# Kernel tuning notes

Hardware: AMD Instinct MI355X
Metric: run time of the kernel (lower is better)

The kernel has to match this reference:

```python
import jax, jax.numpy as jnp
import numpy as np

C = 512
NUM_GROUPS = 32
EPS = 1e-6


def setup_inputs() -> dict:
    key = jax.random.key(0)
    ks = jax.random.split(key, 6)
    B, H, W = 4, 64, 64
    x = jax.random.normal(ks[0], (B, H, W, C), dtype=jnp.float32)
    # GroupNorm affine params (flax default init: scale=1, bias=0)
    gn_scale = jnp.ones((C,), jnp.float32)
    gn_bias = jnp.zeros((C,), jnp.float32)
    # 1x1 convs == per-pixel dense layers; weight [C_in, C_out], bias [C_out]
    def dense(k):
        return jax.random.normal(k, (C, C), dtype=jnp.float32) * 0.02
    wq, wk, wv, wo = dense(ks[1]), dense(ks[2]), dense(ks[3]), dense(ks[4])
    bq = jnp.zeros((C,), jnp.float32)
    bk = jnp.zeros((C,), jnp.float32)
    bv = jnp.zeros((C,), jnp.float32)
    bo = jnp.zeros((C,), jnp.float32)
    return {"x": x, "gn_scale": gn_scale, "gn_bias": gn_bias,
            "wq": wq, "bq": bq, "wk": wk, "bk": bk,
            "wv": wv, "bv": bv, "wo": wo, "bo": bo}


def _group_norm(x, scale, bias):
    B, H, W, Cc = x.shape
    g = NUM_GROUPS
    xg = x.reshape(B, H, W, g, Cc // g)
    mean = jnp.mean(xg, axis=(1, 2, 4), keepdims=True)
    var = jnp.var(xg, axis=(1, 2, 4), keepdims=True)
    xn = (xg - mean) * jax.lax.rsqrt(var + EPS)
    xn = xn.reshape(B, H, W, Cc)
    return xn * scale + bias


def reference(x, gn_scale, gn_bias, wq, bq, wk, bk, wv, bv, wo, bo):
    B, H, W, Cc = x.shape
    hn = _group_norm(x, gn_scale, gn_bias)
    # 1x1 convs
    q = (hn @ wq + bq).reshape(B, H * W, Cc)
    k = (hn @ wk + bk).reshape(B, H * W, Cc)
    v = (hn @ wv + bv).reshape(B, H * W, Cc)
    scale = jnp.asarray(Cc, x.dtype) ** -0.5
    # scores[b,i,j] = <q_i, k_j> * c^-0.5; softmax over keys j
    attn = jax.nn.softmax(jnp.einsum('bic,bjc->bij', q, k) * scale, axis=-1)
    out = jnp.einsum('bij,bjc->bic', attn, v).reshape(B, H, W, Cc)
    return x + (out @ wo + bo)
```

## Files before the change

kernel.cpp:

```cpp
#include <hip/hip_runtime.h>


typedef __attribute__((ext_vector_type(8))) __bf16 bf16x8;
typedef __attribute__((ext_vector_type(4))) __bf16 bf16x4;
typedef __attribute__((ext_vector_type(4))) float  floatx4;

#define C_DIM 512
#define SPB   4096
#define MTOT  16384

#define HN_OFF  ((size_t)0)
#define Q_OFF   ((size_t)16 << 20)
#define K_OFF   ((size_t)32 << 20)
#define V4_OFF  ((size_t)48 << 20)
#define WT_OFF  ((size_t)64 << 20)
#define O1_OFF  ((size_t)68 << 20)
#define ML_OFF  ((size_t)84 << 20)
#define GS_OFF  (ML_OFF + (size_t)(256 << 10))

__device__ inline floatx4 mfma16(bf16x8 a, bf16x8 b, floatx4 c) {
    return __builtin_amdgcn_mfma_f32_16x16x32_bf16(a, b, c, 0, 0, 0);
}

__device__ inline void gload16(const void* g, void* lds) {
    __builtin_amdgcn_global_load_lds(
        (const __attribute__((address_space(1))) unsigned int*)g,
        (__attribute__((address_space(3))) unsigned int*)lds, 16, 0, 0);
}

__global__ __launch_bounds__(256) void zero_stats(float* gstats) {
    gstats[threadIdx.x] = 0.f;
}

__global__ __launch_bounds__(256) void gn_stats(
    const float* __restrict__ x, float* __restrict__ gstats,
    __bf16* __restrict__ xb) {
    int bg = blockIdx.x;
    int b = bg >> 5, g = bg & 31;
    int tid = threadIdx.x;
    int cq = tid & 3, s0 = tid >> 2;
    size_t off = (size_t)b * SPB * C_DIM + g * 16 + cq * 4
               + (size_t)blockIdx.y * 1024 * C_DIM;
    const float* base = x + off;
    __bf16* xbb = xb + off;
    float sum = 0.f, sq = 0.f;
#pragma unroll 4
    for (int i = 0; i < 16; ++i) {
        floatx4 v = *(const floatx4*)(base + (size_t)(i * 64 + s0) * C_DIM);
        sum += v[0] + v[1] + v[2] + v[3];
        sq  += v[0]*v[0] + v[1]*v[1] + v[2]*v[2] + v[3]*v[3];
        bf16x4 o;
#pragma unroll
        for (int j = 0; j < 4; ++j) o[j] = (__bf16)v[j];
        *(bf16x4*)(xbb + (size_t)(i * 64 + s0) * C_DIM) = o;
    }
#pragma unroll
    for (int off2 = 1; off2 < 64; off2 <<= 1) {
        sum += __shfl_xor(sum, off2);
        sq  += __shfl_xor(sq,  off2);
    }
    __shared__ float sm[8];
    int w = tid >> 6, lane = tid & 63;
    if (lane == 0) { sm[w] = sum; sm[4 + w] = sq; }
    __syncthreads();
    if (tid == 0) {
        atomicAdd(&gstats[bg * 2],     sm[0] + sm[1] + sm[2] + sm[3]);
        atomicAdd(&gstats[bg * 2 + 1], sm[4] + sm[5] + sm[6] + sm[7]);
    }
}

__global__ __launch_bounds__(256) void gn_apply(
    const __bf16* __restrict__ xb, const float* __restrict__ gstats,
    const float* __restrict__ gsc, const float* __restrict__ gbi,
    __bf16* __restrict__ hn) {
    int bg = blockIdx.x;
    int b = bg >> 5, g = bg & 31;
    int tid = threadIdx.x;
    int cq = tid & 3, s0 = tid >> 2;
    float S  = gstats[bg * 2], Qs = gstats[bg * 2 + 1];
    float mean = S * (1.f / 65536.f);
    float var  = Qs * (1.f / 65536.f) - mean * mean;
    float rstd = rsqrtf(var + 1e-6f);
    float sc[4], bi[4];
#pragma unroll
    for (int j = 0; j < 4; ++j) {
        float s_ = gsc[g * 16 + cq * 4 + j] * rstd;
        sc[j] = s_;
        bi[j] = gbi[g * 16 + cq * 4 + j] - mean * s_;
    }
    size_t off = (size_t)b * SPB * C_DIM + g * 16 + cq * 4
               + (size_t)blockIdx.y * 1024 * C_DIM;
    const __bf16* base = xb + off;
    __bf16* hbase = hn + off;
#pragma unroll 4
    for (int i = 0; i < 16; ++i) {
        bf16x4 v = *(const bf16x4*)(base + (size_t)(i * 64 + s0) * C_DIM);
        bf16x4 o;
#pragma unroll
        for (int j = 0; j < 4; ++j) o[j] = (__bf16)((float)v[j] * sc[j] + bi[j]);
        *(bf16x4*)(hbase + (size_t)(i * 64 + s0) * C_DIM) = o;
    }
}

__global__ __launch_bounds__(256) void wt_kernel(
    const float* __restrict__ w0, const float* __restrict__ w1,
    const float* __restrict__ w2, const float* __restrict__ w3,
    __bf16* __restrict__ wt) {
    const float* srcs[4] = {w0, w1, w2, w3};
    const float* src = srcs[blockIdx.z];
    __bf16* dst = wt + (size_t)blockIdx.z * C_DIM * C_DIM;
    __shared__ float tile[32][33];
    int tx = threadIdx.x & 31, ty = threadIdx.x >> 5;
    int gx = blockIdx.x * 32, gy = blockIdx.y * 32;
#pragma unroll
    for (int i = 0; i < 4; ++i)
        tile[ty + i * 8][tx] = src[(size_t)(gy + ty + i * 8) * C_DIM + gx + tx];
    __syncthreads();
#pragma unroll
    for (int i = 0; i < 4; ++i) {
        int n = gx + ty + i * 8;
        int k = gy + tx;
        dst[(size_t)n * C_DIM + k] = (__bf16)tile[tx][ty + i * 8];
    }
}

__global__ __launch_bounds__(256, 2) void proj_qkv(
    const __bf16* __restrict__ hn, const __bf16* __restrict__ wt_all,
    const float* __restrict__ bq, const float* __restrict__ bk,
    const float* __restrict__ bv, __bf16* __restrict__ qout,
    __bf16* __restrict__ kout, __bf16* __restrict__ v4out) {
    int z = blockIdx.z;
    const __bf16* wt = wt_all + (size_t)z * C_DIM * C_DIM;
    const float* bias = (z == 0) ? bq : (z == 1) ? bk : bv;
    __shared__ __bf16 Alds[128 * 32];
    __shared__ __bf16 Blds[128 * 32];
    int tid = threadIdx.x, lane = tid & 63, w = tid >> 6;
    int c = lane & 15, quad = lane >> 4;
    int wm = w & 1, wn = w >> 1;
    int mbase = blockIdx.x * 128, nbase = blockIdx.y * 128;
    floatx4 acc[4][4] = {};
    for (int kb = 0; kb < 16; ++kb) {
        __syncthreads();
#pragma unroll
        for (int p = 0; p < 2; ++p) {
            int chunk0 = w * 128 + p * 64;
            int chunk = chunk0 + lane;
            int row = chunk >> 2, qk = chunk & 3;
            gload16(hn + (size_t)(mbase + row) * C_DIM + kb * 32 + qk * 8, Alds + chunk0 * 8);
            gload16(wt + (size_t)(nbase + row) * C_DIM + kb * 32 + qk * 8, Blds + chunk0 * 8);
        }
        __syncthreads();
        bf16x8 af[4], bfr[4];
#pragma unroll
        for (int mt = 0; mt < 4; ++mt)
            af[mt] = *(const bf16x8*)(Alds + (wm * 64 + mt * 16 + c) * 32 + quad * 8);
#pragma unroll
        for (int nt = 0; nt < 4; ++nt)
            bfr[nt] = *(const bf16x8*)(Blds + (wn * 64 + nt * 16 + c) * 32 + quad * 8);
#pragma unroll
        for (int mt = 0; mt < 4; ++mt)
#pragma unroll
            for (int nt = 0; nt < 4; ++nt)
                acc[mt][nt] = mfma16(af[mt], bfr[nt], acc[mt][nt]);
    }
    float scale = (z == 0) ? 0.0441941738241592f : 1.0f;
#pragma unroll
    for (int nt = 0; nt < 4; ++nt) {
        int n = nbase + wn * 64 + nt * 16 + c;
        float bval = bias[n];
#pragma unroll
        for (int mt = 0; mt < 4; ++mt) {
            int m0 = mbase + wm * 64 + mt * 16 + quad * 4;
#pragma unroll
            for (int r = 0; r < 4; ++r) {
                int m = m0 + r;
                float val = (acc[mt][nt][r] + bval) * scale;
                if (z == 0)      qout[(size_t)m * C_DIM + n] = (__bf16)val;
                else if (z == 1) kout[(size_t)m * C_DIM + n] = (__bf16)val;
                else {
                    int bb = m >> 12, pos = m & 4095;
                    v4out[((size_t)(bb * 512 + (pos >> 3)) * C_DIM + n) * 8 + (pos & 7)] = (__bf16)val;
                }
            }
        }
    }
}

__device__ inline void stage_K(const __bf16* kbase, int key0,
                               __bf16* Kl, int w, int lane) {
#pragma unroll
    for (int p = 0; p < 8; ++p) {
        int chunk0 = w * 512 + p * 64;
        int chunk = chunk0 + lane;
        gload16(kbase + (size_t)(key0 + (chunk & 31)) * C_DIM + (chunk >> 5) * 8,
                Kl + chunk0 * 8);
    }
}

__global__ __launch_bounds__(256, 2) void flash_kernel(
    const __bf16* __restrict__ q, const __bf16* __restrict__ kmat,
    const __bf16* __restrict__ v4, __bf16* __restrict__ op0,
    __bf16* __restrict__ op1, float* __restrict__ lpart) {
    __shared__ __bf16 Klds[2][16384];
    __shared__ __bf16 Plds[2][64 * 40];
    int tid = threadIdx.x, lane = tid & 63, w = tid >> 6;
    int c = lane & 15, quad = lane >> 4;
    int bid = blockIdx.x;
    int combo = bid & 7;
    int b = combo >> 1, h = combo & 1, qt = bid >> 3;
    int hk = h * 2048;
    int wch = w * 128;

    const __bf16* qp = q + ((size_t)(b * SPB + qt * 64 + w * 16 + c)) * C_DIM + quad * 8;
    bf16x8 qf[16];
#pragma unroll
    for (int ks = 0; ks < 16; ++ks) qf[ks] = *(const bf16x8*)(qp + ks * 32);
    floatx4 o[4][8];
#pragma unroll
    for (int mg = 0; mg < 4; ++mg)
#pragma unroll
        for (int t = 0; t < 8; ++t) o[mg][t] = (floatx4){0.f, 0.f, 0.f, 0.f};
    float l_r[4] = {0.f, 0.f, 0.f, 0.f};

    const __bf16* kbase = kmat + (size_t)b * SPB * C_DIM;
    const __bf16* vbase = v4 + (size_t)b * 512 * C_DIM * 8;

    stage_K(kbase, hk,      &Klds[0][0], w, lane);
    stage_K(kbase, hk + 32, &Klds[1][0], w, lane);
    __syncthreads();

    for (int kt = 0; kt < 64; ++kt) {
        int KB = kt & 1;
        const __bf16* KL = &Klds[KB][0];
        __bf16* PL = &Plds[KB][0];
        const __bf16* vp = vbase + ((size_t)(((hk + kt * 32) >> 3) + quad) * 512 + wch + c) * 8;
        bf16x8 v0 = *(const bf16x8*)(vp);
        bf16x8 v1 = *(const bf16x8*)(vp + 16 * 8);
        bf16x8 v2 = *(const bf16x8*)(vp + 32 * 8);
        bf16x8 v3 = *(const bf16x8*)(vp + 48 * 8);
        bf16x8 v4r = *(const bf16x8*)(vp + 64 * 8);
        bf16x8 v5 = *(const bf16x8*)(vp + 80 * 8);
        bf16x8 v6 = *(const bf16x8*)(vp + 96 * 8);
        bf16x8 v7 = *(const bf16x8*)(vp + 112 * 8);
        floatx4 s0 = (floatx4){0.f,0.f,0.f,0.f}, s1 = (floatx4){0.f,0.f,0.f,0.f};
#pragma unroll
        for (int ks = 0; ks < 16; ++ks) {
            bf16x8 k0 = *(const bf16x8*)(KL + (((ks * 4 + quad) * 32) + c) * 8);
            bf16x8 k1 = *(const bf16x8*)(KL + (((ks * 4 + quad) * 32) + c + 16) * 8);
            s0 = mfma16(qf[ks], k0, s0);
            s1 = mfma16(qf[ks], k1, s1);
        }
#pragma unroll
        for (int r = 0; r < 4; ++r) {
            float p0 = __expf(s0[r]);
            float p1 = __expf(s1[r]);
            l_r[r] += p0 + p1;
            int row = w * 16 + quad * 4 + r;
            PL[row * 40 + c]      = (__bf16)p0;
            PL[row * 40 + c + 16] = (__bf16)p1;
        }
        __syncthreads();
        if (kt < 62) stage_K(kbase, hk + (kt + 2) * 32, &Klds[KB][0], w, lane);
        bf16x8 pf[4];
#pragma unroll
        for (int mg = 0; mg < 4; ++mg)
            pf[mg] = *(const bf16x8*)(PL + (mg * 16 + c) * 40 + quad * 8);
#pragma unroll
        for (int mg = 0; mg < 4; ++mg) {
            o[mg][0] = mfma16(pf[mg], v0, o[mg][0]);
            o[mg][1] = mfma16(pf[mg], v1, o[mg][1]);
            o[mg][2] = mfma16(pf[mg], v2, o[mg][2]);
            o[mg][3] = mfma16(pf[mg], v3, o[mg][3]);
            o[mg][4] = mfma16(pf[mg], v4r, o[mg][4]);
            o[mg][5] = mfma16(pf[mg], v5, o[mg][5]);
            o[mg][6] = mfma16(pf[mg], v6, o[mg][6]);
            o[mg][7] = mfma16(pf[mg], v7, o[mg][7]);
        }
    }
#pragma unroll
    for (int r = 0; r < 4; ++r) {
        float l = l_r[r];
        l += __shfl_xor(l, 1);
        l += __shfl_xor(l, 2);
        l += __shfl_xor(l, 4);
        l += __shfl_xor(l, 8);
        l_r[r] = l;
    }
    if (c == 0) {
#pragma unroll
        for (int r = 0; r < 4; ++r) {
            int grow = b * SPB + qt * 64 + w * 16 + quad * 4 + r;
            lpart[h * MTOT + grow] = l_r[r];
        }
    }
    __bf16* ob = h ? op1 : op0;
#pragma unroll
    for (int mg = 0; mg < 4; ++mg)
#pragma unroll
        for (int t = 0; t < 8; ++t)
#pragma unroll
            for (int r = 0; r < 4; ++r) {
                int grow = b * SPB + qt * 64 + mg * 16 + quad * 4 + r;
                ob[(size_t)grow * C_DIM + wch + t * 16 + c] = (__bf16)o[mg][t][r];
            }
}

__global__ __launch_bounds__(256, 2) void proj_out(
    const __bf16* __restrict__ o0, const __bf16* __restrict__ o1,
    const float* __restrict__ lp, const __bf16* __restrict__ wot,
    const float* __restrict__ bo, const float* __restrict__ x,
    float* __restrict__ out) {
    __shared__ __bf16 Alds[128 * 32];
    __shared__ __bf16 Blds[128 * 32];
    __shared__ float linv[128];
    int tid = threadIdx.x, lane = tid & 63, w = tid >> 6;
    int c = lane & 15, quad = lane >> 4;
    int wm = w & 1, wn = w >> 1;
    int mbase = blockIdx.x * 128, nbase = blockIdx.y * 128;
    if (tid < 128) {
        int row = mbase + tid;
        linv[tid] = 1.f / (lp[row] + lp[MTOT + row]);
    }
    floatx4 acc[4][4] = {};
    for (int kb = 0; kb < 16; ++kb) {
        __syncthreads();
#pragma unroll
        for (int p = 0; p < 2; ++p) {
            int chunk = tid + p * 256;
            int row = chunk >> 2, qk = chunk & 3;
            size_t gidx = (size_t)(mbase + row) * C_DIM + kb * 32 + qk * 8;
            bf16x8 a0 = *(const bf16x8*)(o0 + gidx);
            bf16x8 a1 = *(const bf16x8*)(o1 + gidx);
            float s = linv[row];
            bf16x8 rr;
#pragma unroll
            for (int j = 0; j < 8; ++j)
                rr[j] = (__bf16)(((float)a0[j] + (float)a1[j]) * s);
            *(bf16x8*)(Alds + chunk * 8) = rr;
        }
#pragma unroll
        for (int p = 0; p < 2; ++p) {
            int chunk0 = w * 128 + p * 64;
            int chunk = chunk0 + lane;
            int row = chunk >> 2, qk = chunk & 3;
            gload16(wot + (size_t)(nbase + row) * C_DIM + kb * 32 + qk * 8, Blds + chunk0 * 8);
        }
        __syncthreads();
        bf16x8 af[4], bfr[4];
#pragma unroll
        for (int mt = 0; mt < 4; ++mt)
            af[mt] = *(const bf16x8*)(Alds + (wm * 64 + mt * 16 + c) * 32 + quad * 8);
#pragma unroll
        for (int nt = 0; nt < 4; ++nt)
            bfr[nt] = *(const bf16x8*)(Blds + (wn * 64 + nt * 16 + c) * 32 + quad * 8);
#pragma unroll
        for (int mt = 0; mt < 4; ++mt)
#pragma unroll
            for (int nt = 0; nt < 4; ++nt)
                acc[mt][nt] = mfma16(af[mt], bfr[nt], acc[mt][nt]);
    }
#pragma unroll
    for (int nt = 0; nt < 4; ++nt) {
        int n = nbase + wn * 64 + nt * 16 + c;
        float bval = bo[n];
#pragma unroll
        for (int mt = 0; mt < 4; ++mt) {
            int m0 = mbase + wm * 64 + mt * 16 + quad * 4;
#pragma unroll
            for (int r = 0; r < 4; ++r) {
                size_t idx = (size_t)(m0 + r) * C_DIM + n;
                out[idx] = acc[mt][nt][r] + bval + x[idx];
            }
        }
    }
}

extern "C" void kernel_launch(void* const* d_in, const int* in_sizes, int n_in,
                              void* d_out, int out_size, void* d_ws, size_t ws_size,
                              hipStream_t stream) {
    const float* x   = (const float*)d_in[0];
    const float* gsc = (const float*)d_in[1];
    const float* gbi = (const float*)d_in[2];
    const float* wq  = (const float*)d_in[3];
    const float* bq  = (const float*)d_in[4];
    const float* wk  = (const float*)d_in[5];
    const float* bk  = (const float*)d_in[6];
    const float* wv  = (const float*)d_in[7];
    const float* bv  = (const float*)d_in[8];
    const float* wo  = (const float*)d_in[9];
    const float* bo  = (const float*)d_in[10];
    char* ws = (char*)d_ws;
    __bf16* hn  = (__bf16*)(ws + HN_OFF);
    __bf16* qb  = (__bf16*)(ws + Q_OFF);
    __bf16* kb  = (__bf16*)(ws + K_OFF);
    __bf16* v4  = (__bf16*)(ws + V4_OFF);
    __bf16* wt  = (__bf16*)(ws + WT_OFF);
    __bf16* op0 = (__bf16*)(ws + HN_OFF);
    __bf16* op1 = (__bf16*)(ws + O1_OFF);
    __bf16* xb  = (__bf16*)(ws + O1_OFF);
    float*  lp  = (float*)(ws + ML_OFF);
    float*  gs  = (float*)(ws + GS_OFF);
    float* out = (float*)d_out;

    zero_stats<<<1, 256, 0, stream>>>(gs);
    wt_kernel<<<dim3(16, 16, 4), 256, 0, stream>>>(wq, wk, wv, wo, wt);
    gn_stats<<<dim3(128, 4), 256, 0, stream>>>(x, gs, xb);
    gn_apply<<<dim3(128, 4), 256, 0, stream>>>(xb, gs, gsc, gbi, hn);
    proj_qkv<<<dim3(128, 4, 3), 256, 0, stream>>>(hn, wt, bq, bk, bv, qb, kb, v4);
    flash_kernel<<<512, 256, 0, stream>>>(qb, kb, v4, op0, op1, lp);
    proj_out<<<dim3(128, 4), 256, 0, stream>>>(op0, op1, lp,
        wt + (size_t)3 * C_DIM * C_DIM, bo, x, out);
}
```

Measured before the change: 479.5 us.

## Use single-buffered 64-key K tiles with permuted key layout in flash loop

The attention loop now handles 64 keys per iteration with one LDS K buffer instead of 32-key double-buffered tiles. Keys are stored in a permuted order so each lane's four score values land in consecutive P columns and can be written with one vector store. This halves the number of loop iterations and barrier pairs per block. In exchange, a second barrier per iteration is added and the async prefetch of the next K tile now overlaps only with the PV phase, which may expose load latency.

```diff
diff --git a/kernel.cpp b/kernel.cpp
--- a/kernel.cpp
+++ b/kernel.cpp
@@ -186,14 +186,15 @@
     }
 }
 
-__device__ inline void stage_K(const __bf16* kbase, int key0,
-                               __bf16* Kl, int w, int lane) {
-#pragma unroll
-    for (int p = 0; p < 8; ++p) {
-        int chunk0 = w * 512 + p * 64;
+__device__ inline void stage_K64(const __bf16* kbase, int key0,
+                                 __bf16* Kl, int w, int lane) {
+#pragma unroll
+    for (int p = 0; p < 16; ++p) {
+        int chunk0 = w * 1024 + p * 64;
         int chunk = chunk0 + lane;
-        gload16(kbase + (size_t)(key0 + (chunk & 31)) * C_DIM + (chunk >> 5) * 8,
-                Kl + chunk0 * 8);
+        int cg = chunk >> 6, slot = chunk & 63;
+        int key = ((slot & 15) << 2) + (slot >> 4);
+        gload16(kbase + (size_t)(key0 + key) * C_DIM + cg * 8, Kl + chunk0 * 8);
     }
 }
 
@@ -201,8 +202,8 @@
     const __bf16* __restrict__ q, const __bf16* __restrict__ kmat,
     const __bf16* __restrict__ v4, __bf16* __restrict__ op0,
     __bf16* __restrict__ op1, float* __restrict__ lpart) {
-    __shared__ __bf16 Klds[2][16384];
-    __shared__ __bf16 Plds[2][64 * 40];
+    __shared__ __bf16 Klds[64 * 64 * 8];
+    __shared__ __bf16 Plds[64 * 72];
     int tid = threadIdx.x, lane = tid & 63, w = tid >> 6;
     int c = lane & 15, quad = lane >> 4;
     int bid = blockIdx.x;
@@ -225,57 +226,62 @@
     const __bf16* kbase = kmat + (size_t)b * SPB * C_DIM;
     const __bf16* vbase = v4 + (size_t)b * 512 * C_DIM * 8;
 
-    stage_K(kbase, hk,      &Klds[0][0], w, lane);
-    stage_K(kbase, hk + 32, &Klds[1][0], w, lane);
+    stage_K64(kbase, hk, Klds, w, lane);
     __syncthreads();
 
-    for (int kt = 0; kt < 64; ++kt) {
-        int KB = kt & 1;
-        const __bf16* KL = &Klds[KB][0];
-        __bf16* PL = &Plds[KB][0];
-        const __bf16* vp = vbase + ((size_t)(((hk + kt * 32) >> 3) + quad) * 512 + wch + c) * 8;
-        bf16x8 v0 = *(const bf16x8*)(vp);
-        bf16x8 v1 = *(const bf16x8*)(vp + 16 * 8);
-        bf16x8 v2 = *(const bf16x8*)(vp + 32 * 8);
-        bf16x8 v3 = *(const bf16x8*)(vp + 48 * 8);
-        bf16x8 v4r = *(const bf16x8*)(vp + 64 * 8);
-        bf16x8 v5 = *(const bf16x8*)(vp + 80 * 8);
-        bf16x8 v6 = *(const bf16x8*)(vp + 96 * 8);
-        bf16x8 v7 = *(const bf16x8*)(vp + 112 * 8);
-        floatx4 s0 = (floatx4){0.f,0.f,0.f,0.f}, s1 = (floatx4){0.f,0.f,0.f,0.f};
+    for (int kt = 0; kt < 32; ++kt) {
+        int key0 = hk + kt * 64;
+        floatx4 s0 = (floatx4){0.f,0.f,0.f,0.f}, s1 = s0, s2 = s0, s3 = s0;
 #pragma unroll
         for (int ks = 0; ks < 16; ++ks) {
-            bf16x8 k0 = *(const bf16x8*)(KL + (((ks * 4 + quad) * 32) + c) * 8);
-            bf16x8 k1 = *(const bf16x8*)(KL + (((ks * 4 + quad) * 32) + c + 16) * 8);
-            s0 = mfma16(qf[ks], k0, s0);
-            s1 = mfma16(qf[ks], k1, s1);
+            const __bf16* kb_ = Klds + (size_t)(ks * 4 + quad) * 64 * 8;
+            s0 = mfma16(qf[ks], *(const bf16x8*)(kb_ + (c)      * 8), s0);
+            s1 = mfma16(qf[ks], *(const bf16x8*)(kb_ + (c + 16) * 8), s1);
+            s2 = mfma16(qf[ks], *(const bf16x8*)(kb_ + (c + 32) * 8), s2);
+            s3 = mfma16(qf[ks], *(const bf16x8*)(kb_ + (c + 48) * 8), s3);
         }
 #pragma unroll
         for (int r = 0; r < 4; ++r) {
             float p0 = __expf(s0[r]);
             float p1 = __expf(s1[r]);
-            l_r[r] += p0 + p1;
+            float p2 = __expf(s2[r]);
+            float p3 = __expf(s3[r]);
+            l_r[r] += (p0 + p1) + (p2 + p3);
             int row = w * 16 + quad * 4 + r;
-            PL[row * 40 + c]      = (__bf16)p0;
-            PL[row * 40 + c + 16] = (__bf16)p1;
-        }
-        __syncthreads();
-        if (kt < 62) stage_K(kbase, hk + (kt + 2) * 32, &Klds[KB][0], w, lane);
-        bf16x8 pf[4];
-#pragma unroll
-        for (int mg = 0; mg < 4; ++mg)
-            pf[mg] = *(const bf16x8*)(PL + (mg * 16 + c) * 40 + quad * 8);
-#pragma unroll
-        for (int mg = 0; mg < 4; ++mg) {
-            o[mg][0] = mfma16(pf[mg], v0, o[mg][0]);
-            o[mg][1] = mfma16(pf[mg], v1, o[mg][1]);
-            o[mg][2] = mfma16(pf[mg], v2, o[mg][2]);
-            o[mg][3] = mfma16(pf[mg], v3, o[mg][3]);
-            o[mg][4] = mfma16(pf[mg], v4r, o[mg][4]);
-            o[mg][5] = mfma16(pf[mg], v5, o[mg][5]);
-            o[mg][6] = mfma16(pf[mg], v6, o[mg][6]);
-            o[mg][7] = mfma16(pf[mg], v7, o[mg][7]);
-        }
+            bf16x4 pk = {(__bf16)p0, (__bf16)p1, (__bf16)p2, (__bf16)p3};
+            *(bf16x4*)(Plds + row * 72 + c * 4) = pk;
+        }
+        __syncthreads();
+        if (kt < 31) stage_K64(kbase, key0 + 64, Klds, w, lane);
+#pragma unroll
+        for (int half = 0; half < 2; ++half) {
+            const __bf16* vp = vbase
+                + ((size_t)(((key0 + half * 32) >> 3) + quad) * 512 + wch + c) * 8;
+            bf16x8 vf0 = *(const bf16x8*)(vp);
+            bf16x8 vf1 = *(const bf16x8*)(vp + 16 * 8);
+            bf16x8 vf2 = *(const bf16x8*)(vp + 32 * 8);
+            bf16x8 vf3 = *(const bf16x8*)(vp + 48 * 8);
+            bf16x8 vf4 = *(const bf16x8*)(vp + 64 * 8);
+            bf16x8 vf5 = *(const bf16x8*)(vp + 80 * 8);
+            bf16x8 vf6 = *(const bf16x8*)(vp + 96 * 8);
+            bf16x8 vf7 = *(const bf16x8*)(vp + 112 * 8);
+            bf16x8 pf[4];
+#pragma unroll
+            for (int mg = 0; mg < 4; ++mg)
+                pf[mg] = *(const bf16x8*)(Plds + (mg * 16 + c) * 72 + half * 32 + quad * 8);
+#pragma unroll
+            for (int mg = 0; mg < 4; ++mg) {
+                o[mg][0] = mfma16(pf[mg], vf0, o[mg][0]);
+                o[mg][1] = mfma16(pf[mg], vf1, o[mg][1]);
+                o[mg][2] = mfma16(pf[mg], vf2, o[mg][2]);
+                o[mg][3] = mfma16(pf[mg], vf3, o[mg][3]);
+                o[mg][4] = mfma16(pf[mg], vf4, o[mg][4]);
+                o[mg][5] = mfma16(pf[mg], vf5, o[mg][5]);
+                o[mg][6] = mfma16(pf[mg], vf6, o[mg][6]);
+                o[mg][7] = mfma16(pf[mg], vf7, o[mg][7]);
+            }
+        }
+        __syncthreads();
     }
 #pragma unroll
     for (int r = 0; r < 4; ++r) {
```

New measurement: 446.9 us. -6.8%, faster.
